# Performance work log

Hardware: AMD Instinct MI355X
Metric: run time of the kernel (lower is better)

The kernel has to match this reference:

```python
import jax, jax.numpy as jnp
import numpy as np

VOCAB = 50000
D_EMB = 300
N_BINS = 11
B, LQ, LD = 64, 32, 1024
MU = np.array([1.0, 0.9, 0.7, 0.5, 0.3, 0.1, -0.1, -0.3, -0.5, -0.7, -0.9], dtype=np.float32)
SIGMA = np.array([1e-3] + [0.1] * 10, dtype=np.float32)


def setup_inputs() -> dict:
    key = jax.random.key(0)
    ks = jax.random.split(key, 8)
    inputs_q = jax.random.randint(ks[0], (B, LQ), 0, VOCAB, dtype=jnp.int64 if jax.config.jax_enable_x64 else jnp.int32)
    inputs_d = jax.random.randint(ks[1], (B, LD), 0, VOCAB, dtype=jnp.int64 if jax.config.jax_enable_x64 else jnp.int32)
    mask_q = jnp.ones((B, LQ), dtype=jnp.float32)
    mask_d = jnp.ones((B, LD), dtype=jnp.float32)
    word_emb = jax.random.normal(ks[2], (VOCAB, D_EMB), dtype=jnp.float32) * 0.1
    attn_table = jax.random.uniform(ks[3], (VOCAB, 1), dtype=jnp.float32)  # frozen IDF embedding
    idf_w = jax.random.normal(ks[4], (1, 1), dtype=jnp.float32)
    idf_b = jnp.zeros((1,), dtype=jnp.float32)
    dense_w = jax.random.normal(ks[5], (1, N_BINS), dtype=jnp.float32) * 0.1
    dense_b = jnp.zeros((1,), dtype=jnp.float32)
    return {
        'inputs_q': inputs_q, 'inputs_d': inputs_d,
        'mask_q': mask_q, 'mask_d': mask_d,
        'word_emb': word_emb, 'attn_table': attn_table,
        'idf_w': idf_w, 'idf_b': idf_b,
        'dense_w': dense_w, 'dense_b': dense_b,
    }


def _l2_normalize(x, eps=1e-12):
    # matches F.normalize(x, 2, dim=-1): x / max(||x||, eps)
    n = jnp.sqrt(jnp.sum(x * x, axis=-1, keepdims=True))
    return x / jnp.maximum(n, eps)


def reference(inputs_q, inputs_d, mask_q, mask_d, word_emb, attn_table,
              idf_w, idf_b, dense_w, dense_b):
    mu = jnp.asarray(MU)        # [K]
    sigma = jnp.asarray(SIGMA)  # [K]
    # idf attention on query tokens: Linear(1,1) on frozen embedding lookup
    attn_q = attn_table[inputs_q] * idf_w[0, 0] + idf_b[0]          # [B,Lq,1]
    q_embed = _l2_normalize(word_emb[inputs_q])                      # [B,Lq,E]
    d_embed = _l2_normalize(word_emb[inputs_d])                      # [B,Ld,E]
    sim = jnp.einsum('bqe,bde->bqd', q_embed, d_embed)               # [B,Lq,Ld]
    # RBF soft-histogram over n_bins kernels, doc tokens masked
    rbf = jnp.exp(-((sim[..., None] - mu) ** 2) / (sigma ** 2) / 2)  # [B,Lq,Ld,K]
    pooling_sum = jnp.einsum('bqdk,bd->bqk', rbf, mask_d)            # [B,Lq,K]
    wq = mask_q[..., None] * attn_q                                   # [B,Lq,1]
    log_pool = jnp.log(jnp.clip(pooling_sum, 1e-10)) * wq * 0.01     # [B,Lq,K]
    log_pooling_sum = jnp.sum(log_pool, axis=1)                      # [B,K]
    out = jnp.tanh(log_pooling_sum @ dense_w.T + dense_b)            # [B,1]
    return out[:, 0]                                                 # [B]
```

## Files before the change

kernel.cpp:

```cpp
#include <hip/hip_runtime.h>
#include <math.h>

#define VOCAB  50000
#define D_EMB  300
#define NBINS  11
#define BATCH  64
#define LQ     32
#define LD     1024
#define DTILE  64
#define NDT    (LD / DTILE)
#define NSTEP  10
#define KPAD   320

#define PARTIAL_BYTES ((size_t)NDT * BATCH * LQ * NBINS * 4)
#define TB_OFF        PARTIAL_BYTES
#define TB_BYTES      ((size_t)VOCAB * KPAD * 2)
#define INV_OFF       (TB_OFF + TB_BYTES)
#define INV_BYTES     ((size_t)VOCAB * 4)
#define WS_NEED       (INV_OFF + INV_BYTES)

typedef __attribute__((ext_vector_type(8))) short short8;
typedef __attribute__((ext_vector_type(4))) float floatx4;
typedef __attribute__((ext_vector_type(4))) unsigned short us4;
typedef unsigned int u32;

__constant__ float c_mu[NBINS]  = {1.0f, 0.9f, 0.7f, 0.5f, 0.3f, 0.1f,
                                   -0.1f, -0.3f, -0.5f, -0.7f, -0.9f};
__constant__ float c_is2[NBINS] = {500000.0f, 50.f, 50.f, 50.f, 50.f, 50.f,
                                   50.f, 50.f, 50.f, 50.f, 50.f};

static __device__ __forceinline__ unsigned short f32_bf16(float f) {
  unsigned u = __float_as_uint(f);
  u += 0x7FFFu + ((u >> 16) & 1u);
  return (unsigned short)(u >> 16);
}
static __device__ __forceinline__ float bf16_f32(unsigned short h) {
  return __uint_as_float(((unsigned)h) << 16);
}

static __device__ __forceinline__ void gload_lds16(const void* g, void* l) {
  __builtin_amdgcn_global_load_lds(
      (__attribute__((address_space(1))) u32*)g,
      (__attribute__((address_space(3))) u32*)l, 16, 0, 0);
}

__global__ __launch_bounds__(256) void knrm_prep(
    const float* __restrict__ word_emb,
    unsigned short* __restrict__ tb, float* __restrict__ invn)
{
  const int wid  = threadIdx.x >> 6;
  const int lane = threadIdx.x & 63;
  const int row  = blockIdx.x * 4 + wid;
  if (row >= VOCAB) return;
  const float4* src = (const float4*)(word_emb + (size_t)row * D_EMB);
  const float4 a = src[lane];
  float4 c = make_float4(0.f, 0.f, 0.f, 0.f);
  if (lane < 11) c = src[64 + lane];
  us4 ha, hc;
  ha.x = f32_bf16(a.x); ha.y = f32_bf16(a.y);
  ha.z = f32_bf16(a.z); ha.w = f32_bf16(a.w);
  hc.x = f32_bf16(c.x); hc.y = f32_bf16(c.y);
  hc.z = f32_bf16(c.z); hc.w = f32_bf16(c.w);
  float p = 0.f;
  { float x;
    x = bf16_f32(ha.x); p += x * x;  x = bf16_f32(ha.y); p += x * x;
    x = bf16_f32(ha.z); p += x * x;  x = bf16_f32(ha.w); p += x * x;
    x = bf16_f32(hc.x); p += x * x;  x = bf16_f32(hc.y); p += x * x;
    x = bf16_f32(hc.z); p += x * x;  x = bf16_f32(hc.w); p += x * x; }
#pragma unroll
  for (int off = 1; off < 64; off <<= 1) p += __shfl_xor(p, off);
  unsigned short* orow = tb + (size_t)row * KPAD;
  *(us4*)(orow + 4 * lane) = ha;
  if (lane < 16) *(us4*)(orow + 256 + 4 * lane) = hc;
  if (lane == 0) invn[row] = 1.f / fmaxf(sqrtf(p), 1e-12f);
}

__global__ __launch_bounds__(256) void knrm_main(
    const int* __restrict__ inputs_q, const int* __restrict__ inputs_d,
    const float* __restrict__ mask_d, const unsigned short* __restrict__ tb,
    const float* __restrict__ invn, float* __restrict__ partial)
{
  const int b    = blockIdx.y;
  const int dt   = blockIdx.x;
  const int tid  = threadIdx.x;
  const int wid  = tid >> 6;
  const int lane = tid & 63;
  const int khi  = lane >> 4;
  const int rl   = lane & 15;

  __shared__ __align__(16) short Afrag[2 * NSTEP * 512];
  __shared__ __align__(16) short Bfrag[4 * NSTEP * 512];
  __shared__ float invq_s[LQ], invd_s[DTILE], maskd_s[DTILE];
  __shared__ float red[4][16][NBINS];

  const int dbase = b * LD + dt * DTILE;

  int tokX, tokY, ybase;
  short *dstX, *dstY;
  if (wid == 0)      { tokX = inputs_q[b * LQ + rl];        dstX = Afrag;
                       tokY = inputs_d[dbase + rl];         dstY = Bfrag;                  ybase = 0; }
  else if (wid == 1) { tokX = inputs_q[b * LQ + 16 + rl];   dstX = Afrag + NSTEP * 512;
                       tokY = inputs_d[dbase + rl];         dstY = Bfrag;                  ybase = 5; }
  else if (wid == 2) { tokX = inputs_d[dbase + 16 + rl];    dstX = Bfrag + NSTEP * 512;
                       tokY = inputs_d[dbase + 32 + rl];    dstY = Bfrag + 2 * NSTEP * 512; ybase = 0; }
  else               { tokX = inputs_d[dbase + 48 + rl];    dstX = Bfrag + 3 * NSTEP * 512;
                       tokY = inputs_d[dbase + 32 + rl];    dstY = Bfrag + 2 * NSTEP * 512; ybase = 5; }

  const char* srcX = (const char*)(tb + (size_t)tokX * KPAD) + khi * 16;
  const char* srcY = (const char*)(tb + (size_t)tokY * KPAD) + khi * 16;
#pragma unroll
  for (int s = 0; s < NSTEP; ++s)
    gload_lds16(srcX + 64 * s, dstX + s * 512);
#pragma unroll
  for (int s = 0; s < 5; ++s)
    gload_lds16(srcY + 64 * (ybase + s), dstY + (ybase + s) * 512);

  if (tid < LQ)      invq_s[tid] = invn[inputs_q[b * LQ + tid]];
  else if (tid < 96) { const int d = tid - 32;
                       invd_s[d]  = invn[inputs_d[dbase + d]];
                       maskd_s[d] = mask_d[dbase + d]; }
  __syncthreads();

  const int qt = wid >> 1, dp = wid & 1;
  const short* Ab = Afrag + qt * NSTEP * 512;
  const short* B0 = Bfrag + (2 * dp) * NSTEP * 512;
  const short* B1 = Bfrag + (2 * dp + 1) * NSTEP * 512;
  floatx4 acc0 = {0.f, 0.f, 0.f, 0.f};
  floatx4 acc1 = {0.f, 0.f, 0.f, 0.f};
#pragma unroll
  for (int s = 0; s < NSTEP; ++s) {
    const short8 a  = *(const short8*)(Ab + s * 512 + lane * 8);
    const short8 b0 = *(const short8*)(B0 + s * 512 + lane * 8);
    const short8 b1 = *(const short8*)(B1 + s * 512 + lane * 8);
    acc0 = __builtin_amdgcn_mfma_f32_16x16x32_bf16(a, b0, acc0, 0, 0, 0);
    acc1 = __builtin_amdgcn_mfma_f32_16x16x32_bf16(a, b1, acc1, 0, 0, 0);
  }

  float ps[4][NBINS];
#pragma unroll
  for (int r = 0; r < 4; ++r)
#pragma unroll
    for (int k = 0; k < NBINS; ++k) ps[r][k] = 0.f;

  float iq[4];
#pragma unroll
  for (int r = 0; r < 4; ++r) iq[r] = invq_s[16 * qt + 4 * khi + r];

#pragma unroll
  for (int t = 0; t < 2; ++t) {
    const int   dl = 32 * dp + 16 * t + rl;
    const float id = invd_s[dl];
    const float md = maskd_s[dl];
    const floatx4 acc = t ? acc1 : acc0;
#pragma unroll
    for (int r = 0; r < 4; ++r) {
      const float sv = acc[r] * iq[r] * id;
#pragma unroll
      for (int k = 0; k < NBINS; ++k) {
        const float d = sv - c_mu[k];
        ps[r][k] += md * __expf(-d * d * c_is2[k]);
      }
    }
  }

#pragma unroll
  for (int off = 1; off < 16; off <<= 1)
#pragma unroll
    for (int r = 0; r < 4; ++r)
#pragma unroll
      for (int k = 0; k < NBINS; ++k)
        ps[r][k] += __shfl_xor(ps[r][k], off);

  if (rl == 0)
#pragma unroll
    for (int r = 0; r < 4; ++r)
#pragma unroll
      for (int k = 0; k < NBINS; ++k)
        red[wid][4 * khi + r][k] = ps[r][k];
  __syncthreads();

  float* pout = partial + ((size_t)dt * BATCH + b) * (LQ * NBINS);
  for (int v = tid; v < LQ * NBINS; v += 256) {
    const int q = v / NBINS, k = v % NBINS;
    pout[v] = (q < 16) ? (red[0][q][k] + red[1][q][k])
                       : (red[2][q - 16][k] + red[3][q - 16][k]);
  }
}

static __device__ __forceinline__ float stage_rows(
    const float* __restrict__ emb_row, short* __restrict__ region,
    int s_begin, int s_end, int khi, int lane)
{
  const float4* emb4 = (const float4*)emb_row;
  float p = 0.f;
  for (int s = s_begin; s < s_end; ++s) {
    const int k0 = 32 * s + 8 * khi;
    float4 fa = make_float4(0.f, 0.f, 0.f, 0.f);
    float4 fb = make_float4(0.f, 0.f, 0.f, 0.f);
    if (k0 < D_EMB)     fa = emb4[k0 >> 2];
    if (k0 + 4 < D_EMB) fb = emb4[(k0 >> 2) + 1];
    unsigned short h[8];
    h[0] = f32_bf16(fa.x); h[1] = f32_bf16(fa.y);
    h[2] = f32_bf16(fa.z); h[3] = f32_bf16(fa.w);
    h[4] = f32_bf16(fb.x); h[5] = f32_bf16(fb.y);
    h[6] = f32_bf16(fb.z); h[7] = f32_bf16(fb.w);
    short8 v;
#pragma unroll
    for (int j = 0; j < 8; ++j) {
      const float x = bf16_f32(h[j]);
      p += x * x;
      v[j] = (short)h[j];
    }
    *(short8*)(region + s * 512 + lane * 8) = v;
  }
  return p;
}

__global__ __launch_bounds__(256) void knrm_main_fb(
    const int* __restrict__ inputs_q, const int* __restrict__ inputs_d,
    const float* __restrict__ mask_d, const float* __restrict__ word_emb,
    float* __restrict__ partial)
{
  const int b    = blockIdx.y;
  const int dt   = blockIdx.x;
  const int tid  = threadIdx.x;
  const int wid  = tid >> 6;
  const int lane = tid & 63;
  const int khi  = lane >> 4;
  const int rl   = lane & 15;

  __shared__ __align__(16) short Afrag[2 * NSTEP * 512];
  __shared__ __align__(16) short Bfrag[4 * NSTEP * 512];
  __shared__ float sumsq_s[96];
  __shared__ float invq_s[LQ], invd_s[DTILE], maskd_s[DTILE];
  __shared__ float red[4][16][NBINS];

  if (tid < 96) sumsq_s[tid] = 0.f;
  if (tid < DTILE) maskd_s[tid] = mask_d[b * LD + dt * DTILE + tid];
  __syncthreads();

  {
    int tok; float p;
    if (wid == 0) {
      tok = inputs_q[b * LQ + rl];
      p = stage_rows(word_emb + (size_t)tok * D_EMB, Afrag, 0, NSTEP, khi, lane);
      p += __shfl_xor(p, 16); p += __shfl_xor(p, 32);
      if (lane < 16) atomicAdd(&sumsq_s[lane], p);
      tok = inputs_d[b * LD + dt * DTILE + rl];
      p = stage_rows(word_emb + (size_t)tok * D_EMB, Bfrag, 0, 5, khi, lane);
      p += __shfl_xor(p, 16); p += __shfl_xor(p, 32);
      if (lane < 16) atomicAdd(&sumsq_s[32 + lane], p);
    } else if (wid == 1) {
      tok = inputs_q[b * LQ + 16 + rl];
      p = stage_rows(word_emb + (size_t)tok * D_EMB, Afrag + NSTEP * 512, 0, NSTEP, khi, lane);
      p += __shfl_xor(p, 16); p += __shfl_xor(p, 32);
      if (lane < 16) atomicAdd(&sumsq_s[16 + lane], p);
      tok = inputs_d[b * LD + dt * DTILE + rl];
      p = stage_rows(word_emb + (size_t)tok * D_EMB, Bfrag, 5, NSTEP, khi, lane);
      p += __shfl_xor(p, 16); p += __shfl_xor(p, 32);
      if (lane < 16) atomicAdd(&sumsq_s[32 + lane], p);
    } else if (wid == 2) {
      tok = inputs_d[b * LD + dt * DTILE + 16 + rl];
      p = stage_rows(word_emb + (size_t)tok * D_EMB, Bfrag + NSTEP * 512, 0, NSTEP, khi, lane);
      p += __shfl_xor(p, 16); p += __shfl_xor(p, 32);
      if (lane < 16) atomicAdd(&sumsq_s[48 + lane], p);
      tok = inputs_d[b * LD + dt * DTILE + 32 + rl];
      p = stage_rows(word_emb + (size_t)tok * D_EMB, Bfrag + 2 * NSTEP * 512, 0, 5, khi, lane);
      p += __shfl_xor(p, 16); p += __shfl_xor(p, 32);
      if (lane < 16) atomicAdd(&sumsq_s[64 + lane], p);
    } else {
      tok = inputs_d[b * LD + dt * DTILE + 48 + rl];
      p = stage_rows(word_emb + (size_t)tok * D_EMB, Bfrag + 3 * NSTEP * 512, 0, NSTEP, khi, lane);
      p += __shfl_xor(p, 16); p += __shfl_xor(p, 32);
      if (lane < 16) atomicAdd(&sumsq_s[80 + lane], p);
      tok = inputs_d[b * LD + dt * DTILE + 32 + rl];
      p = stage_rows(word_emb + (size_t)tok * D_EMB, Bfrag + 2 * NSTEP * 512, 5, NSTEP, khi, lane);
      p += __shfl_xor(p, 16); p += __shfl_xor(p, 32);
      if (lane < 16) atomicAdd(&sumsq_s[64 + lane], p);
    }
  }
  __syncthreads();

  if (tid < 96) {
    const float s   = sumsq_s[tid];
    const float inv = 1.f / fmaxf(sqrtf(s), 1e-12f);
    if (tid < 32) invq_s[tid] = inv; else invd_s[tid - 32] = inv;
  }
  __syncthreads();

  const int qt = wid >> 1, dp = wid & 1;
  const short* Ab = Afrag + qt * NSTEP * 512;
  const short* B0 = Bfrag + (2 * dp) * NSTEP * 512;
  const short* B1 = Bfrag + (2 * dp + 1) * NSTEP * 512;
  floatx4 acc0 = {0.f, 0.f, 0.f, 0.f};
  floatx4 acc1 = {0.f, 0.f, 0.f, 0.f};
#pragma unroll
  for (int s = 0; s < NSTEP; ++s) {
    const short8 a  = *(const short8*)(Ab + s * 512 + lane * 8);
    const short8 b0 = *(const short8*)(B0 + s * 512 + lane * 8);
    const short8 b1 = *(const short8*)(B1 + s * 512 + lane * 8);
    acc0 = __builtin_amdgcn_mfma_f32_16x16x32_bf16(a, b0, acc0, 0, 0, 0);
    acc1 = __builtin_amdgcn_mfma_f32_16x16x32_bf16(a, b1, acc1, 0, 0, 0);
  }

  float ps[4][NBINS];
#pragma unroll
  for (int r = 0; r < 4; ++r)
#pragma unroll
    for (int k = 0; k < NBINS; ++k) ps[r][k] = 0.f;

  float iq[4];
#pragma unroll
  for (int r = 0; r < 4; ++r) iq[r] = invq_s[16 * qt + 4 * khi + r];

#pragma unroll
  for (int t = 0; t < 2; ++t) {
    const int   dl = 32 * dp + 16 * t + rl;
    const float id = invd_s[dl];
    const float md = maskd_s[dl];
    const floatx4 acc = t ? acc1 : acc0;
#pragma unroll
    for (int r = 0; r < 4; ++r) {
      const float sv = acc[r] * iq[r] * id;
#pragma unroll
      for (int k = 0; k < NBINS; ++k) {
        const float d = sv - c_mu[k];
        ps[r][k] += md * __expf(-d * d * c_is2[k]);
      }
    }
  }

#pragma unroll
  for (int off = 1; off < 16; off <<= 1)
#pragma unroll
    for (int r = 0; r < 4; ++r)
#pragma unroll
      for (int k = 0; k < NBINS; ++k)
        ps[r][k] += __shfl_xor(ps[r][k], off);

  if (rl == 0)
#pragma unroll
    for (int r = 0; r < 4; ++r)
#pragma unroll
      for (int k = 0; k < NBINS; ++k)
        red[wid][4 * khi + r][k] = ps[r][k];
  __syncthreads();

  float* pout = partial + ((size_t)dt * BATCH + b) * (LQ * NBINS);
  for (int v = tid; v < LQ * NBINS; v += 256) {
    const int q = v / NBINS, k = v % NBINS;
    pout[v] = (q < 16) ? (red[0][q][k] + red[1][q][k])
                       : (red[2][q - 16][k] + red[3][q - 16][k]);
  }
}

__global__ __launch_bounds__(128) void knrm_finalize(
    const float* __restrict__ partial, const int* __restrict__ inputs_q,
    const float* __restrict__ mask_q, const float* __restrict__ attn_table,
    const float* __restrict__ idf_w, const float* __restrict__ idf_b,
    const float* __restrict__ dense_w, const float* __restrict__ dense_b,
    float* __restrict__ out)
{
  const int b   = blockIdx.x;
  const int tid = threadIdx.x;
  __shared__ float pool[LQ][NBINS];
  __shared__ float wq_s[LQ];
  __shared__ float lps[NBINS];

  for (int v = tid; v < LQ * NBINS; v += 128) {
    float s = 0.f;
#pragma unroll
    for (int t = 0; t < NDT; ++t)
      s += partial[((size_t)t * BATCH + b) * (LQ * NBINS) + v];
    pool[v / NBINS][v % NBINS] = logf(fmaxf(s, 1e-10f));
  }
  if (tid < LQ) {
    const int tok = inputs_q[b * LQ + tid];
    wq_s[tid] = mask_q[b * LQ + tid] * (attn_table[tok] * idf_w[0] + idf_b[0]);
  }
  __syncthreads();
  if (tid < NBINS) {
    float s = 0.f;
    for (int q = 0; q < LQ; ++q) s += pool[q][tid] * wq_s[q];
    lps[tid] = 0.01f * s;
  }
  __syncthreads();
  if (tid == 0) {
    float z = dense_b[0];
    for (int k = 0; k < NBINS; ++k) z += lps[k] * dense_w[k];
    out[b] = tanhf(z);
  }
}

extern "C" void kernel_launch(void* const* d_in, const int* in_sizes, int n_in,
                              void* d_out, int out_size, void* d_ws, size_t ws_size,
                              hipStream_t stream) {
  const int*   inputs_q  = (const int*)d_in[0];
  const int*   inputs_d  = (const int*)d_in[1];
  const float* mask_q    = (const float*)d_in[2];
  const float* mask_d    = (const float*)d_in[3];
  const float* word_emb  = (const float*)d_in[4];
  const float* attn_tab  = (const float*)d_in[5];
  const float* idf_w     = (const float*)d_in[6];
  const float* idf_b     = (const float*)d_in[7];
  const float* dense_w   = (const float*)d_in[8];
  const float* dense_b   = (const float*)d_in[9];
  float* out     = (float*)d_out;
  float* partial = (float*)d_ws;

  dim3 grid(NDT, BATCH);
  if (ws_size >= WS_NEED) {
    unsigned short* tb = (unsigned short*)((char*)d_ws + TB_OFF);
    float* invn        = (float*)((char*)d_ws + INV_OFF);
    knrm_prep<<<VOCAB / 4, 256, 0, stream>>>(word_emb, tb, invn);
    knrm_main<<<grid, 256, 0, stream>>>(inputs_q, inputs_d, mask_d, tb, invn, partial);
  } else {
    knrm_main_fb<<<grid, 256, 0, stream>>>(inputs_q, inputs_d, mask_d, word_emb, partial);
  }
  knrm_finalize<<<BATCH, 128, 0, stream>>>(partial, inputs_q, mask_q, attn_tab,
                                           idf_w, idf_b, dense_w, dense_b, out);
}
```

Baseline: 136.7 us.

## Drop full-vocab bf16 conversion; convert gathered doc rows in-kernel and prepack queries

The old path converted the entire 50k-row embedding table to bf16 on every call, even though only the tokens actually used are needed. Now a small prep kernel converts only the query rows into MFMA-ready fragments with their inverse norms. The main kernel gathers fp32 doc rows directly into swizzled LDS, converts them to bf16 in registers and computes their norms itself. Doc tiles shrink from 64 to 32 rows, which doubles the grid and the number of partial sums the finalize kernel must reduce, and the fp32 gather moves twice the bytes per doc row.

Result: slower. 163.7 us (+19.8%).

```diff
diff --git a/kernel.cpp b/kernel.cpp
--- a/kernel.cpp
+++ b/kernel.cpp
@@ -7,21 +7,21 @@
 #define BATCH  64
 #define LQ     32
 #define LD     1024
+#define NSTEP  10
+
+#define DT2    32
+#define NDT2   (LD / DT2)
 #define DTILE  64
 #define NDT    (LD / DTILE)
-#define NSTEP  10
-#define KPAD   320
-
-#define PARTIAL_BYTES ((size_t)NDT * BATCH * LQ * NBINS * 4)
-#define TB_OFF        PARTIAL_BYTES
-#define TB_BYTES      ((size_t)VOCAB * KPAD * 2)
-#define INV_OFF       (TB_OFF + TB_BYTES)
-#define INV_BYTES     ((size_t)VOCAB * 4)
-#define WS_NEED       (INV_OFF + INV_BYTES)
+
+#define PARTIAL2_BYTES ((size_t)NDT2 * BATCH * LQ * NBINS * 4)
+#define QTAB_OFF       PARTIAL2_BYTES
+#define QTAB_BYTES     ((size_t)BATCH * 2 * NSTEP * 512 * 2)
+#define INVQ_OFF       ((size_t)4194304)
+#define WS_NEED2       (INVQ_OFF + (size_t)BATCH * LQ * 4)
 
 typedef __attribute__((ext_vector_type(8))) short short8;
 typedef __attribute__((ext_vector_type(4))) float floatx4;
-typedef __attribute__((ext_vector_type(4))) unsigned short us4;
 typedef unsigned int u32;
 
 __constant__ float c_mu[NBINS]  = {1.0f, 0.9f, 0.7f, 0.5f, 0.3f, 0.1f,
@@ -44,41 +44,51 @@
       (__attribute__((address_space(3))) u32*)l, 16, 0, 0);
 }
 
-__global__ __launch_bounds__(256) void knrm_prep(
-    const float* __restrict__ word_emb,
-    unsigned short* __restrict__ tb, float* __restrict__ invn)
+__global__ __launch_bounds__(256) void knrm_qprep(
+    const int* __restrict__ inputs_q, const float* __restrict__ word_emb,
+    unsigned short* __restrict__ qtab, float* __restrict__ invq)
 {
   const int wid  = threadIdx.x >> 6;
   const int lane = threadIdx.x & 63;
-  const int row  = blockIdx.x * 4 + wid;
-  if (row >= VOCAB) return;
-  const float4* src = (const float4*)(word_emb + (size_t)row * D_EMB);
-  const float4 a = src[lane];
-  float4 c = make_float4(0.f, 0.f, 0.f, 0.f);
-  if (lane < 11) c = src[64 + lane];
-  us4 ha, hc;
-  ha.x = f32_bf16(a.x); ha.y = f32_bf16(a.y);
-  ha.z = f32_bf16(a.z); ha.w = f32_bf16(a.w);
-  hc.x = f32_bf16(c.x); hc.y = f32_bf16(c.y);
-  hc.z = f32_bf16(c.z); hc.w = f32_bf16(c.w);
+  const int qi   = blockIdx.x * 4 + wid;
+  const int tok  = inputs_q[qi];
+  const int b    = qi >> 5, q = qi & 31;
+  const int rl   = q & 15, qt = q >> 4;
+
+  const float4* src = (const float4*)(word_emb + (size_t)tok * D_EMB);
+  float4 fa = make_float4(0.f, 0.f, 0.f, 0.f);
+  float4 fb = make_float4(0.f, 0.f, 0.f, 0.f);
+  if (lane < 38) fa = src[2 * lane];
+  if (lane < 37) fb = src[2 * lane + 1];
+
+  unsigned short h[8];
+  h[0] = f32_bf16(fa.x); h[1] = f32_bf16(fa.y);
+  h[2] = f32_bf16(fa.z); h[3] = f32_bf16(fa.w);
+  h[4] = f32_bf16(fb.x); h[5] = f32_bf16(fb.y);
+  h[6] = f32_bf16(fb.z); h[7] = f32_bf16(fb.w);
   float p = 0.f;
-  { float x;
-    x = bf16_f32(ha.x); p += x * x;  x = bf16_f32(ha.y); p += x * x;
-    x = bf16_f32(ha.z); p += x * x;  x = bf16_f32(ha.w); p += x * x;
-    x = bf16_f32(hc.x); p += x * x;  x = bf16_f32(hc.y); p += x * x;
-    x = bf16_f32(hc.z); p += x * x;  x = bf16_f32(hc.w); p += x * x; }
+  short8 v;
+#pragma unroll
+  for (int j = 0; j < 8; ++j) {
+    const float x = bf16_f32(h[j]);
+    p += x * x;
+    v[j] = (short)h[j];
+  }
 #pragma unroll
   for (int off = 1; off < 64; off <<= 1) p += __shfl_xor(p, off);
-  unsigned short* orow = tb + (size_t)row * KPAD;
-  *(us4*)(orow + 4 * lane) = ha;
-  if (lane < 16) *(us4*)(orow + 256 + 4 * lane) = hc;
-  if (lane == 0) invn[row] = 1.f / fmaxf(sqrtf(p), 1e-12f);
-}
-
-__global__ __launch_bounds__(256) void knrm_main(
-    const int* __restrict__ inputs_q, const int* __restrict__ inputs_d,
-    const float* __restrict__ mask_d, const unsigned short* __restrict__ tb,
-    const float* __restrict__ invn, float* __restrict__ partial)
+  if (lane == 0) invq[qi] = 1.f / fmaxf(sqrtf(p), 1e-12f);
+
+  if (lane < 40) {
+    const int s = lane >> 2, khi = lane & 3;
+    *(short8*)(qtab + ((size_t)(b * 2 + qt)) * (NSTEP * 512)
+                    + s * 512 + (khi * 16 + rl) * 8) = v;
+  }
+}
+
+__global__ __launch_bounds__(256) void knrm_main2(
+    const int* __restrict__ inputs_d, const float* __restrict__ mask_d,
+    const float* __restrict__ word_emb, const unsigned short* __restrict__ qtab,
+    const float* __restrict__ invq, float* __restrict__ partial)
 {
   const int b    = blockIdx.y;
   const int dt   = blockIdx.x;
@@ -89,51 +99,77 @@
   const int rl   = lane & 15;
 
   __shared__ __align__(16) short Afrag[2 * NSTEP * 512];
-  __shared__ __align__(16) short Bfrag[4 * NSTEP * 512];
-  __shared__ float invq_s[LQ], invd_s[DTILE], maskd_s[DTILE];
+  __shared__ __align__(16) float Dstage[DT2 * 320];
+  __shared__ float invq_s[LQ];
   __shared__ float red[4][16][NBINS];
 
-  const int dbase = b * LD + dt * DTILE;
-
-  int tokX, tokY, ybase;
-  short *dstX, *dstY;
-  if (wid == 0)      { tokX = inputs_q[b * LQ + rl];        dstX = Afrag;
-                       tokY = inputs_d[dbase + rl];         dstY = Bfrag;                  ybase = 0; }
-  else if (wid == 1) { tokX = inputs_q[b * LQ + 16 + rl];   dstX = Afrag + NSTEP * 512;
-                       tokY = inputs_d[dbase + rl];         dstY = Bfrag;                  ybase = 5; }
-  else if (wid == 2) { tokX = inputs_d[dbase + 16 + rl];    dstX = Bfrag + NSTEP * 512;
-                       tokY = inputs_d[dbase + 32 + rl];    dstY = Bfrag + 2 * NSTEP * 512; ybase = 0; }
-  else               { tokX = inputs_d[dbase + 48 + rl];    dstX = Bfrag + 3 * NSTEP * 512;
-                       tokY = inputs_d[dbase + 32 + rl];    dstY = Bfrag + 2 * NSTEP * 512; ybase = 5; }
-
-  const char* srcX = (const char*)(tb + (size_t)tokX * KPAD) + khi * 16;
-  const char* srcY = (const char*)(tb + (size_t)tokY * KPAD) + khi * 16;
-#pragma unroll
-  for (int s = 0; s < NSTEP; ++s)
-    gload_lds16(srcX + 64 * s, dstX + s * 512);
-#pragma unroll
-  for (int s = 0; s < 5; ++s)
-    gload_lds16(srcY + 64 * (ybase + s), dstY + (ybase + s) * 512);
-
-  if (tid < LQ)      invq_s[tid] = invn[inputs_q[b * LQ + tid]];
-  else if (tid < 96) { const int d = tid - 32;
-                       invd_s[d]  = invn[inputs_d[dbase + d]];
-                       maskd_s[d] = mask_d[dbase + d]; }
+  const int dbase = b * LD + dt * DT2;
+
+  {
+    char* Dst = (char*)Dstage;
+    const char* embb = (const char*)word_emb;
+#pragma unroll
+    for (int i = 0; i < 10; ++i) {
+      const int obase = (wid * 10 + i) * 1024;
+      const int o = obase + lane * 16;
+      const int r = (o >> 8) / 5;
+      int bo = (o - r * 1280) ^ ((r & 7) << 4);
+      if (bo >= 1200) bo = 0;
+      const int tok = inputs_d[dbase + r];
+      gload_lds16(embb + (size_t)tok * 1200 + bo, Dst + obase);
+    }
+  }
+  {
+    const char* qsrc = (const char*)(qtab + (size_t)b * 2 * (NSTEP * 512));
+    char* Adst = (char*)Afrag;
+#pragma unroll
+    for (int i = 0; i < 5; ++i) {
+      const int off = (wid * 5 + i) * 1024;
+      gload_lds16(qsrc + off + lane * 16, Adst + off);
+    }
+  }
+  if (tid < LQ) invq_s[tid] = invq[b * LQ + tid];
   __syncthreads();
 
   const int qt = wid >> 1, dp = wid & 1;
-  const short* Ab = Afrag + qt * NSTEP * 512;
-  const short* B0 = Bfrag + (2 * dp) * NSTEP * 512;
-  const short* B1 = Bfrag + (2 * dp + 1) * NSTEP * 512;
-  floatx4 acc0 = {0.f, 0.f, 0.f, 0.f};
-  floatx4 acc1 = {0.f, 0.f, 0.f, 0.f};
+  const int rloc = dp * 16 + rl;
+  short8 bfr[NSTEP];
+  float p = 0.f;
+  {
+    const char* rowp = (const char*)Dstage + rloc * 1280;
+    const int swz = (rloc & 7) << 4;
+#pragma unroll
+    for (int s = 0; s < NSTEP; ++s) {
+      const int k0 = 32 * s + 8 * khi;
+      const int c0 = 4 * k0;
+      float4 fa = make_float4(0.f, 0.f, 0.f, 0.f);
+      float4 fb = make_float4(0.f, 0.f, 0.f, 0.f);
+      if (k0 < D_EMB)     fa = *(const float4*)(rowp + (c0 ^ swz));
+      if (k0 + 4 < D_EMB) fb = *(const float4*)(rowp + ((c0 + 16) ^ swz));
+      unsigned short h[8];
+      h[0] = f32_bf16(fa.x); h[1] = f32_bf16(fa.y);
+      h[2] = f32_bf16(fa.z); h[3] = f32_bf16(fa.w);
+      h[4] = f32_bf16(fb.x); h[5] = f32_bf16(fb.y);
+      h[6] = f32_bf16(fb.z); h[7] = f32_bf16(fb.w);
+      short8 v;
+#pragma unroll
+      for (int j = 0; j < 8; ++j) {
+        const float x = bf16_f32(h[j]);
+        p += x * x;
+        v[j] = (short)h[j];
+      }
+      bfr[s] = v;
+    }
+  }
+  p += __shfl_xor(p, 16); p += __shfl_xor(p, 32);
+  const float invd = 1.f / fmaxf(sqrtf(p), 1e-12f);
+
+  const short* Ab = Afrag + qt * (NSTEP * 512);
+  floatx4 acc = {0.f, 0.f, 0.f, 0.f};
 #pragma unroll
   for (int s = 0; s < NSTEP; ++s) {
-    const short8 a  = *(const short8*)(Ab + s * 512 + lane * 8);
-    const short8 b0 = *(const short8*)(B0 + s * 512 + lane * 8);
-    const short8 b1 = *(const short8*)(B1 + s * 512 + lane * 8);
-    acc0 = __builtin_amdgcn_mfma_f32_16x16x32_bf16(a, b0, acc0, 0, 0, 0);
-    acc1 = __builtin_amdgcn_mfma_f32_16x16x32_bf16(a, b1, acc1, 0, 0, 0);
+    const short8 a = *(const short8*)(Ab + s * 512 + lane * 8);
+    acc = __builtin_amdgcn_mfma_f32_16x16x32_bf16(a, bfr[s], acc, 0, 0, 0);
   }
 
   float ps[4][NBINS];
@@ -146,20 +182,14 @@
 #pragma unroll
   for (int r = 0; r < 4; ++r) iq[r] = invq_s[16 * qt + 4 * khi + r];
 
-#pragma unroll
-  for (int t = 0; t < 2; ++t) {
-    const int   dl = 32 * dp + 16 * t + rl;
-    const float id = invd_s[dl];
-    const float md = maskd_s[dl];
-    const floatx4 acc = t ? acc1 : acc0;
-#pragma unroll
-    for (int r = 0; r < 4; ++r) {
-      const float sv = acc[r] * iq[r] * id;
-#pragma unroll
-      for (int k = 0; k < NBINS; ++k) {
-        const float d = sv - c_mu[k];
-        ps[r][k] += md * __expf(-d * d * c_is2[k]);
-      }
+  const float md = mask_d[dbase + rloc];
+#pragma unroll
+  for (int r = 0; r < 4; ++r) {
+    const float sv = acc[r] * iq[r] * invd;
+#pragma unroll
+    for (int k = 0; k < NBINS; ++k) {
+      const float d = sv - c_mu[k];
+      ps[r][k] += md * __expf(-d * d * c_is2[k]);
     }
   }
 
@@ -359,7 +389,7 @@
     const float* __restrict__ mask_q, const float* __restrict__ attn_table,
     const float* __restrict__ idf_w, const float* __restrict__ idf_b,
     const float* __restrict__ dense_w, const float* __restrict__ dense_b,
-    float* __restrict__ out)
+    float* __restrict__ out, int ndt)
 {
   const int b   = blockIdx.x;
   const int tid = threadIdx.x;
@@ -369,8 +399,7 @@
 
   for (int v = tid; v < LQ * NBINS; v += 128) {
     float s = 0.f;
-#pragma unroll
-    for (int t = 0; t < NDT; ++t)
+    for (int t = 0; t < ndt; ++t)
       s += partial[((size_t)t * BATCH + b) * (LQ * NBINS) + v];
     pool[v / NBINS][v % NBINS] = logf(fmaxf(s, 1e-10f));
   }
@@ -408,15 +437,18 @@
   float* out     = (float*)d_out;
   float* partial = (float*)d_ws;
 
-  dim3 grid(NDT, BATCH);
-  if (ws_size >= WS_NEED) {
-    unsigned short* tb = (unsigned short*)((char*)d_ws + TB_OFF);
-    float* invn        = (float*)((char*)d_ws + INV_OFF);
-    knrm_prep<<<VOCAB / 4, 256, 0, stream>>>(word_emb, tb, invn);
-    knrm_main<<<grid, 256, 0, stream>>>(inputs_q, inputs_d, mask_d, tb, invn, partial);
+  if (ws_size >= WS_NEED2) {
+    unsigned short* qtab = (unsigned short*)((char*)d_ws + QTAB_OFF);
+    float* invq          = (float*)((char*)d_ws + INVQ_OFF);
+    knrm_qprep<<<BATCH * LQ / 4, 256, 0, stream>>>(inputs_q, word_emb, qtab, invq);
+    dim3 grid(NDT2, BATCH);
+    knrm_main2<<<grid, 256, 0, stream>>>(inputs_d, mask_d, word_emb, qtab, invq, partial);
+    knrm_finalize<<<BATCH, 128, 0, stream>>>(partial, inputs_q, mask_q, attn_tab,
+                                             idf_w, idf_b, dense_w, dense_b, out, NDT2);
   } else {
+    dim3 grid(NDT, BATCH);
     knrm_main_fb<<<grid, 256, 0, stream>>>(inputs_q, inputs_d, mask_d, word_emb, partial);
-  }
-  knrm_finalize<<<BATCH, 128, 0, stream>>>(partial, inputs_q, mask_q, attn_tab,
-                                           idf_w, idf_b, dense_w, dense_b, out);
-}
+    knrm_finalize<<<BATCH, 128, 0, stream>>>(partial, inputs_q, mask_q, attn_tab,
+                                             idf_w, idf_b, dense_w, dense_b, out, NDT);
+  }
+}
```
